# Kernel tuning notes

Measured on AMD Instinct MI355X. Metric: run time of the kernel, lower is better.

## Reference

```python
import jax, jax.numpy as jnp
import numpy as np

V, E, H, B, S = 50000, 300, 512, 32, 400
SENT_STEP = 20

def _seg_matrix(seq_len, step):
    # PyTorch default: boundaries = range(0, S, step), append S-1 if missing.
    bounds = list(range(0, seq_len, step))
    if bounds[-1] != seq_len - 1:
        bounds.append(seq_len - 1)
    seg = np.searchsorted(np.array(bounds), np.arange(seq_len))  # token -> sentence id
    M = np.zeros((seq_len, len(bounds)), np.float32)
    M[np.arange(seq_len), seg] = 1.0
    M /= M.sum(0, keepdims=True)  # column-normalized -> segment MEAN pooling
    return jnp.asarray(M)

SEG_M = _seg_matrix(S, SENT_STEP)  # [S, n_sent] = [400, 21]

def _gru_dir(x_proj, w_hh, b_hh, reverse):
    # x_proj: [B,T,3H] precomputed x @ W_ih^T + b_ih. PyTorch gate order: r, z, n.
    def step(h, xp):
        gh = h @ w_hh.T + b_hh
        xr, xz, xn = jnp.split(xp, 3, axis=-1)
        hr, hz, hn = jnp.split(gh, 3, axis=-1)
        r = jax.nn.sigmoid(xr + hr)
        z = jax.nn.sigmoid(xz + hz)
        n = jnp.tanh(xn + r * hn)
        h2 = (1.0 - z) * n + z * h
        return h2, h2
    h0 = jnp.zeros((x_proj.shape[0], w_hh.shape[1]), x_proj.dtype)
    h_last, outs = jax.lax.scan(step, h0, x_proj.transpose(1, 0, 2), reverse=reverse)
    return h_last, outs.transpose(1, 0, 2)  # [B,H], [B,T,H]

def _bigru(x, wif, whf, bif, bhf, wib, whb, bib, bhb):
    hf, of = _gru_dir(x @ wif.T + bif, whf, bhf, False)
    hb, ob = _gru_dir(x @ wib.T + bib, whb, bhb, True)
    return jnp.concatenate([of, ob], -1), hf, hb

def setup_inputs():
    key = jax.random.key(0)
    ks = jax.random.split(key, 20)
    f = lambda k, shp: jax.random.normal(k, shp, jnp.float32) * 0.1
    return {
        'input_seq': jax.random.randint(ks[0], (B, S), 0, V),
        'emb': f(ks[1], (V, E)),
        'w_ih_wf': f(ks[2], (3 * H, E)), 'w_hh_wf': f(ks[3], (3 * H, H)),
        'b_ih_wf': f(ks[4], (3 * H,)), 'b_hh_wf': f(ks[5], (3 * H,)),
        'w_ih_wb': f(ks[6], (3 * H, E)), 'w_hh_wb': f(ks[7], (3 * H, H)),
        'b_ih_wb': f(ks[8], (3 * H,)), 'b_hh_wb': f(ks[9], (3 * H,)),
        'w_ih_sf': f(ks[10], (3 * H, 2 * H)), 'w_hh_sf': f(ks[11], (3 * H, H)),
        'b_ih_sf': f(ks[12], (3 * H,)), 'b_hh_sf': f(ks[13], (3 * H,)),
        'w_ih_sb': f(ks[14], (3 * H, 2 * H)), 'w_hh_sb': f(ks[15], (3 * H, H)),
        'b_ih_sb': f(ks[16], (3 * H,)), 'b_hh_sb': f(ks[17], (3 * H,)),
        'fc_w': f(ks[18], (H, 2 * H)), 'fc_b': f(ks[19], (H,)),
    }

def reference(input_seq, emb, w_ih_wf, w_hh_wf, b_ih_wf, b_hh_wf,
              w_ih_wb, w_hh_wb, b_ih_wb, b_hh_wb,
              w_ih_sf, w_hh_sf, b_ih_sf, b_hh_sf,
              w_ih_sb, w_hh_sb, b_ih_sb, b_hh_sb, fc_w, fc_b):
    x = emb[input_seq]  # [B,S,E]; dropout is identity in eval mode
    word_out, _, _ = _bigru(x, w_ih_wf, w_hh_wf, b_ih_wf, b_hh_wf,
                            w_ih_wb, w_hh_wb, b_ih_wb, b_hh_wb)  # [B,S,2H]
    # fused ragged segment-mean pooling (replaces the double python loop)
    sent_rep = jnp.einsum('btd,ts->bsd', word_out, SEG_M)  # [B,n_sent,2H]
    sent_out, hf, hb = _bigru(sent_rep, w_ih_sf, w_hh_sf, b_ih_sf, b_hh_sf,
                              w_ih_sb, w_hh_sb, b_ih_sb, b_hh_sb)
    hidden = jnp.concatenate([hf, hb], -1) @ fc_w.T + fc_b  # [B,H]
    return sent_out, hidden
```

## Files before the change

### kernel.cpp

```cpp
#include <hip/hip_runtime.h>
#include <hip/hip_bf16.h>
#include <hip/hip_cooperative_groups.h>

typedef __bf16 bf16;
typedef __bf16 bf16x4 __attribute__((ext_vector_type(4)));
typedef __bf16 bf16x8 __attribute__((ext_vector_type(8)));
typedef float f32x4 __attribute__((ext_vector_type(4)));

static __device__ __forceinline__ bf16 f2b(float x) { return (bf16)x; }
static __device__ __forceinline__ float b2f(bf16 x) { return (float)x; }

static __device__ __forceinline__ f32x4 mfma16(bf16x8 a, bf16x8 b, f32x4 c) {
  return __builtin_amdgcn_mfma_f32_16x16x32_bf16(a, b, c, 0, 0, 0);
}

static __device__ __forceinline__ bf16x8 loadb8_cc(const bf16* p) {
  bf16x8 v;
  asm volatile("global_load_dwordx4 %0, %1, off sc0 sc1" : "=v"(v) : "v"(p) : "memory");
  return v;
}
static __device__ __forceinline__ void store_b16_cc(bf16* p, bf16 v) {
  unsigned short s;
  __builtin_memcpy(&s, &v, 2);
  unsigned u = s;
  asm volatile("global_store_short %0, %1, off sc0 sc1" :: "v"(p), "v"(u) : "memory");
}

__global__ __launch_bounds__(256) void pad_gather_cvt(
    const float* __restrict__ src, bf16* __restrict__ dst,
    const int* __restrict__ seq, int nrows) {
  int row = blockIdx.x * 4 + (threadIdx.x >> 6);
  int lane = threadIdx.x & 63;
  if (row >= nrows) return;
  int srow;
  if (seq) {
    int s = row >> 5, b = row & 31;
    srow = seq[b * 400 + s];
  } else {
    srow = row;
  }
  const float* sp = src + (size_t)srow * 300;
  bf16* dp = dst + (size_t)row * 320;
  for (int i = lane; i < 320; i += 64) dp[i] = (i < 300) ? f2b(sp[i]) : (bf16)0.f;
}

__global__ __launch_bounds__(256) void cvt_f32_bf16(const float* __restrict__ src,
                                                    bf16* __restrict__ dst,
                                                    int n4) {
  int i = blockIdx.x * 256 + threadIdx.x;
  int stride = gridDim.x * 256;
  for (; i < n4; i += stride) {
    float4 v = ((const float4*)src)[i];
    bf16x4 o = {f2b(v.x), f2b(v.y), f2b(v.z), f2b(v.w)};
    *(bf16x4*)(dst + (size_t)i * 4) = o;
  }
}

__global__ __launch_bounds__(256) void gemm_bt_al(const float* __restrict__ A,
                                                  const bf16* __restrict__ W,
                                                  const float* __restrict__ bias,
                                                  float* __restrict__ C,
                                                  int M, int N, int K) {
  __shared__ bf16 AsH[128][72];
  __shared__ bf16 AsL[128][72];
  __shared__ bf16 Ws[128][72];
  const int n0 = blockIdx.x * 128, m0 = blockIdx.y * 128;
  const int tid = threadIdx.x;
  const int wave = tid >> 6, lane = tid & 63;
  const int l15 = lane & 15, lq = lane >> 4;
  const int wm = (wave >> 1) * 64, wn = (wave & 1) * 64;

  f32x4 acc[4][4] = {};

  for (int k0 = 0; k0 < K; k0 += 64) {
    __syncthreads();
#pragma unroll
    for (int i = 0; i < 8; ++i) {
      int c = tid + 256 * i;
      int r = c >> 4, cc = (c & 15) * 4;
      int gr = m0 + r;
      float4 v = {0.f, 0.f, 0.f, 0.f};
      if (gr < M) v = *(const float4*)(A + (size_t)gr * K + k0 + cc);
      float vv[4] = {v.x, v.y, v.z, v.w};
#pragma unroll
      for (int j = 0; j < 4; ++j) {
        bf16 h = f2b(vv[j]);
        AsH[r][cc + j] = h;
        AsL[r][cc + j] = f2b(vv[j] - b2f(h));
      }
    }
#pragma unroll
    for (int i = 0; i < 4; ++i) {
      int c = tid + 256 * i;
      int r = c >> 3, cc = (c & 7) * 8;
      *(bf16x8*)&Ws[r][cc] = *(const bf16x8*)(W + (size_t)(n0 + r) * K + k0 + cc);
    }
    __syncthreads();
#pragma unroll
    for (int ks = 0; ks < 64; ks += 32) {
      bf16x8 afH[4], afL[4], bfr[4];
#pragma unroll
      for (int i = 0; i < 4; ++i) {
        afH[i] = *(const bf16x8*)&AsH[wm + i * 16 + l15][ks + lq * 8];
        afL[i] = *(const bf16x8*)&AsL[wm + i * 16 + l15][ks + lq * 8];
      }
#pragma unroll
      for (int j = 0; j < 4; ++j)
        bfr[j] = *(const bf16x8*)&Ws[wn + j * 16 + l15][ks + lq * 8];
#pragma unroll
      for (int i = 0; i < 4; ++i)
#pragma unroll
        for (int j = 0; j < 4; ++j) {
          acc[i][j] = mfma16(afH[i], bfr[j], acc[i][j]);
          acc[i][j] = mfma16(afL[i], bfr[j], acc[i][j]);
        }
    }
  }

#pragma unroll
  for (int i = 0; i < 4; ++i)
#pragma unroll
    for (int j = 0; j < 4; ++j) {
      int col = n0 + wn + j * 16 + l15;
      float bv = bias[col];
#pragma unroll
      for (int r = 0; r < 4; ++r) {
        int row = m0 + wm + i * 16 + lq * 4 + r;
        if (row < M) C[(size_t)row * N + col] = acc[i][j][r] + bv;
      }
    }
}

__global__ __launch_bounds__(256) void gru_word(
    const float* __restrict__ whhF, const float* __restrict__ whhB,
    const float* __restrict__ bhhF, const float* __restrict__ bhhB,
    const float* __restrict__ bihF, const float* __restrict__ bihB,
    const bf16* __restrict__ wpad,
    const bf16* __restrict__ xpad,
    bf16* __restrict__ hexb,
    unsigned* __restrict__ flags,
    float* __restrict__ srep)
{
  __shared__ bf16 WlH[48][516];
  __shared__ bf16 WlL[48][516];
  __shared__ bf16 Xw[48][324];
  __shared__ float red[2][4][64][4];
  const int tid = threadIdx.x;
  const int bx = blockIdx.x;
  const int dir = bx >> 5, nb = bx & 31;
  const int c0 = nb * 16;
  const float* whh = dir ? whhB : whhF;
  const float* bhh = dir ? bhhB : bhhF;
  const float* bih = dir ? bihB : bihF;
  const bf16* wih = wpad + (size_t)dir * 1536 * 320;
  unsigned* flg = flags + dir * 32;

#pragma unroll
  for (int i = 0; i < 24; ++i) {
    int c = tid + 256 * i;
    int r = c >> 7, kc = (c & 127) * 4;
    int gr = ((r >> 4) << 9) + c0 + (r & 15);
    float4 v = *(const float4*)(whh + (size_t)gr * 512 + kc);
    float vv[4] = {v.x, v.y, v.z, v.w};
#pragma unroll
    for (int j = 0; j < 4; ++j) {
      bf16 h = f2b(vv[j]);
      WlH[r][kc + j] = h;
      WlL[r][kc + j] = f2b(vv[j] - b2f(h));
    }
  }
#pragma unroll
  for (int i = 0; i < 8; ++i) {
    int c = tid + 256 * i;
    if (c < 1920) {
      int r = c / 40, ch = (c % 40) * 8;
      int gr = ((r >> 4) << 9) + c0 + (r & 15);
      *(bf16x8*)&Xw[r][ch] = *(const bf16x8*)(wih + (size_t)gr * 320 + ch);
    }
  }
  __syncthreads();

  const int wave = tid >> 6, lane = tid & 63;
  const int kh = wave >> 1;
  const int mh = wave & 1;
  const int m0 = mh * 16;
  const int l15 = lane & 15, lq = lane >> 4;
  const int colg = c0 + l15;
  const int rowq = m0 + lq * 4;
  const float bhr = bhh[colg];
  const float bhz = bhh[512 + colg];
  const float bhn = bhh[1024 + colg];
  const float bir = bih[colg];
  const float biz = bih[512 + colg];
  const float bin_ = bih[1024 + colg];

  float pacc0 = 0.f, pacc1 = 0.f, pacc2 = 0.f, pacc3 = 0.f;
  float hp_reg[4] = {0.f, 0.f, 0.f, 0.f};
  bf16* hex_d = hexb + (size_t)dir * 2 * 2 * 16384;

  for (int it = 0; it < 400; ++it) {
    const int t = dir ? (399 - it) : it;
    f32x4 accR = {}, accZ = {}, xN = {}, hN = {};

    {
      const bf16* xrow = xpad + (size_t)(t * 32 + m0 + l15) * 320;
      const int kb = kh * 160;
#pragma unroll
      for (int k0 = 0; k0 < 160; k0 += 32) {
        const int kk = kb + k0 + lq * 8;
        bf16x8 a = *(const bf16x8*)(xrow + kk);
        accR = mfma16(a, *(const bf16x8*)&Xw[l15][kk], accR);
        accZ = mfma16(a, *(const bf16x8*)&Xw[16 + l15][kk], accZ);
        xN = mfma16(a, *(const bf16x8*)&Xw[32 + l15][kk], xN);
      }
    }

    if (it > 0) {
      if (tid < 32) {
        while (__hip_atomic_load(&flg[tid], __ATOMIC_RELAXED,
                                 __HIP_MEMORY_SCOPE_AGENT) < (unsigned)it)
          __builtin_amdgcn_s_sleep(1);
      }
      __syncthreads();

      const bf16* hH = hex_d + (size_t)((it - 1) & 1) * 2 * 16384;
      const bf16* hL = hH + 16384;
      const int rowoff = (m0 + l15) * 512 + kh * 256 + lq * 8;
      bf16x8 hiA[8], loA[8];
#pragma unroll
      for (int c = 0; c < 8; ++c) {
        hiA[c] = loadb8_cc(hH + rowoff + c * 32);
        loA[c] = loadb8_cc(hL + rowoff + c * 32);
      }
      asm volatile("s_waitcnt vmcnt(0)" ::: "memory");
      __builtin_amdgcn_sched_barrier(0);

#pragma unroll
      for (int c = 0; c < 8; ++c) {
        const int kk = kh * 256 + c * 32 + lq * 8;
        bf16x8 wrh = *(const bf16x8*)&WlH[l15][kk];
        bf16x8 wrl = *(const bf16x8*)&WlL[l15][kk];
        bf16x8 wzh = *(const bf16x8*)&WlH[16 + l15][kk];
        bf16x8 wzl = *(const bf16x8*)&WlL[16 + l15][kk];
        bf16x8 wnh = *(const bf16x8*)&WlH[32 + l15][kk];
        bf16x8 wnl = *(const bf16x8*)&WlL[32 + l15][kk];
        accR = mfma16(hiA[c], wrh, accR);
        accR = mfma16(loA[c], wrh, accR);
        accR = mfma16(hiA[c], wrl, accR);
        accZ = mfma16(hiA[c], wzh, accZ);
        accZ = mfma16(loA[c], wzh, accZ);
        accZ = mfma16(hiA[c], wzl, accZ);
        hN = mfma16(hiA[c], wnh, hN);
        hN = mfma16(loA[c], wnh, hN);
        hN = mfma16(hiA[c], wnl, hN);
      }
    }

    if (kh == 0) {
      *(f32x4*)&red[mh][0][lane][0] = accR;
      *(f32x4*)&red[mh][1][lane][0] = accZ;
      *(f32x4*)&red[mh][2][lane][0] = xN;
      *(f32x4*)&red[mh][3][lane][0] = hN;
    }
    __syncthreads();
    if (kh == 1) {
      accR = accR + *(const f32x4*)&red[mh][0][lane][0];
      accZ = accZ + *(const f32x4*)&red[mh][1][lane][0];
      xN = xN + *(const f32x4*)&red[mh][2][lane][0];
      hN = hN + *(const f32x4*)&red[mh][3][lane][0];

      bf16* dH = hex_d + (size_t)(it & 1) * 2 * 16384;
      bf16* dL = dH + 16384;
      float h2v[4];
#pragma unroll
      for (int r = 0; r < 4; ++r) {
        int b = rowq + r;
        float rr = 1.f / (1.f + expf(-(accR[r] + bir + bhr)));
        float zz = 1.f / (1.f + expf(-(accZ[r] + biz + bhz)));
        float nn = tanhf(xN[r] + bin_ + rr * (hN[r] + bhn));
        h2v[r] = (1.f - zz) * nn + zz * hp_reg[r];
        hp_reg[r] = h2v[r];
        bf16 hi = f2b(h2v[r]);
        bf16 lo = f2b(h2v[r] - b2f(hi));
        store_b16_cc(dH + (b << 9) + colg, hi);
        store_b16_cc(dL + (b << 9) + colg, lo);
      }

      int sg = (t == 0) ? 0 : ((t + 19) / 20);
      if (sg > 20) sg = 20;
      float ic = (sg == 0) ? 1.0f : (sg == 20 ? (1.0f / 19.0f) : 0.05f);
      pacc0 += h2v[0] * ic; pacc1 += h2v[1] * ic;
      pacc2 += h2v[2] * ic; pacc3 += h2v[3] * ic;
      bool flush = dir ? (t == 0 || (t % 20) == 1) : ((t % 20) == 0 || t == 399);
      if (flush) {
        float* sp = srep + ((size_t)(sg * 32 + rowq) * 1024) + (dir << 9) + colg;
        sp[0] = pacc0; sp[1024] = pacc1;
        sp[2048] = pacc2; sp[3072] = pacc3;
        pacc0 = pacc1 = pacc2 = pacc3 = 0.f;
      }
    }

    asm volatile("s_waitcnt vmcnt(0)" ::: "memory");
    __syncthreads();
    if (tid == 0)
      __hip_atomic_store(&flg[nb], (unsigned)(it + 1), __ATOMIC_RELAXED,
                         __HIP_MEMORY_SCOPE_AGENT);
  }
}

__global__ __launch_bounds__(256) void gru_sent(
    const float* __restrict__ whhF, const float* __restrict__ whhB,
    const float* __restrict__ bhhF, const float* __restrict__ bhhB,
    const float* __restrict__ xproj,
    bf16* __restrict__ hexb,
    unsigned* __restrict__ flags,
    float* __restrict__ out,
    float* __restrict__ hfin)
{
  __shared__ bf16 WlH[48][516];
  __shared__ bf16 WlL[48][516];
  __shared__ float red[2][3][64][4];
  const int tid = threadIdx.x;
  const int bx = blockIdx.x;
  const int dir = bx >> 5, nb = bx & 31;
  const int c0 = nb * 16;
  const float* whh = dir ? whhB : whhF;
  const float* bhh = dir ? bhhB : bhhF;
  unsigned* flg = flags + dir * 32;

#pragma unroll
  for (int i = 0; i < 24; ++i) {
    int c = tid + 256 * i;
    int r = c >> 7, kc = (c & 127) * 4;
    int gr = ((r >> 4) << 9) + c0 + (r & 15);
    float4 v = *(const float4*)(whh + (size_t)gr * 512 + kc);
    float vv[4] = {v.x, v.y, v.z, v.w};
#pragma unroll
    for (int j = 0; j < 4; ++j) {
      bf16 h = f2b(vv[j]);
      WlH[r][kc + j] = h;
      WlL[r][kc + j] = f2b(vv[j] - b2f(h));
    }
  }
  __syncthreads();

  const int wave = tid >> 6, lane = tid & 63;
  const int kh = wave >> 1;
  const int mh = wave & 1;
  const int m0 = mh * 16;
  const int l15 = lane & 15, lq = lane >> 4;
  const int colg = c0 + l15;
  const int rowq = m0 + lq * 4;
  const float bhr = bhh[colg];
  const float bhz = bhh[512 + colg];
  const float bhn = bhh[1024 + colg];

  float hp_reg[4] = {0.f, 0.f, 0.f, 0.f};
  bf16* hex_d = hexb + (size_t)dir * 2 * 2 * 16384;

  for (int it = 0; it < 21; ++it) {
    const int t = dir ? (20 - it) : it;
    f32x4 accR = {}, accZ = {}, hN = {};

    if (it > 0) {
      if (tid < 32) {
        while (__hip_atomic_load(&flg[tid], __ATOMIC_RELAXED,
                                 __HIP_MEMORY_SCOPE_AGENT) < (unsigned)it)
          __builtin_amdgcn_s_sleep(1);
      }
      __syncthreads();

      const bf16* hH = hex_d + (size_t)((it - 1) & 1) * 2 * 16384;
      const bf16* hL = hH + 16384;
      const int rowoff = (m0 + l15) * 512 + kh * 256 + lq * 8;
      bf16x8 hiA[8], loA[8];
#pragma unroll
      for (int c = 0; c < 8; ++c) {
        hiA[c] = loadb8_cc(hH + rowoff + c * 32);
        loA[c] = loadb8_cc(hL + rowoff + c * 32);
      }
      asm volatile("s_waitcnt vmcnt(0)" ::: "memory");
      __builtin_amdgcn_sched_barrier(0);

#pragma unroll
      for (int c = 0; c < 8; ++c) {
        const int kk = kh * 256 + c * 32 + lq * 8;
        bf16x8 wrh = *(const bf16x8*)&WlH[l15][kk];
        bf16x8 wrl = *(const bf16x8*)&WlL[l15][kk];
        bf16x8 wzh = *(const bf16x8*)&WlH[16 + l15][kk];
        bf16x8 wzl = *(const bf16x8*)&WlL[16 + l15][kk];
        bf16x8 wnh = *(const bf16x8*)&WlH[32 + l15][kk];
        bf16x8 wnl = *(const bf16x8*)&WlL[32 + l15][kk];
        accR = mfma16(hiA[c], wrh, accR);
        accR = mfma16(loA[c], wrh, accR);
        accR = mfma16(hiA[c], wrl, accR);
        accZ = mfma16(hiA[c], wzh, accZ);
        accZ = mfma16(loA[c], wzh, accZ);
        accZ = mfma16(hiA[c], wzl, accZ);
        hN = mfma16(hiA[c], wnh, hN);
        hN = mfma16(loA[c], wnh, hN);
        hN = mfma16(hiA[c], wnl, hN);
      }
    }

    if (kh == 0) {
      *(f32x4*)&red[mh][0][lane][0] = accR;
      *(f32x4*)&red[mh][1][lane][0] = accZ;
      *(f32x4*)&red[mh][2][lane][0] = hN;
    }
    __syncthreads();
    if (kh == 1) {
      accR = accR + *(const f32x4*)&red[mh][0][lane][0];
      accZ = accZ + *(const f32x4*)&red[mh][1][lane][0];
      hN = hN + *(const f32x4*)&red[mh][2][lane][0];

      const float* xp = xproj + ((size_t)dir * 672 + t * 32) * 1536;
      bf16* dH = hex_d + (size_t)(it & 1) * 2 * 16384;
      bf16* dL = dH + 16384;
#pragma unroll
      for (int r = 0; r < 4; ++r) {
        int b = rowq + r;
        float xr = xp[b * 1536 + colg];
        float xz = xp[b * 1536 + 512 + colg];
        float xn = xp[b * 1536 + 1024 + colg];
        float rr = 1.f / (1.f + expf(-(xr + accR[r] + bhr)));
        float zz = 1.f / (1.f + expf(-(xz + accZ[r] + bhz)));
        float nn = tanhf(xn + rr * (hN[r] + bhn));
        float h2 = (1.f - zz) * nn + zz * hp_reg[r];
        hp_reg[r] = h2;
        bf16 hi = f2b(h2);
        bf16 lo = f2b(h2 - b2f(hi));
        store_b16_cc(dH + (b << 9) + colg, hi);
        store_b16_cc(dL + (b << 9) + colg, lo);
        out[(size_t)b * (21 * 1024) + (size_t)t * 1024 + (dir << 9) + colg] = h2;
        if (it == 20) hfin[(dir << 14) + b * 512 + colg] = h2;
      }
    }

    asm volatile("s_waitcnt vmcnt(0)" ::: "memory");
    __syncthreads();
    if (tid == 0)
      __hip_atomic_store(&flg[nb], (unsigned)(it + 1), __ATOMIC_RELAXED,
                         __HIP_MEMORY_SCOPE_AGENT);
  }
}

__global__ __launch_bounds__(256) void fc_k(const float* __restrict__ hfin,
                                            const float* __restrict__ fcw,
                                            const float* __restrict__ fcb,
                                            float* __restrict__ out) {
  __shared__ float hl[1024];
  int b = blockIdx.x, tid = threadIdx.x;
  for (int i = tid; i < 512; i += 256) {
    hl[i] = hfin[b * 512 + i];
    hl[512 + i] = hfin[16384 + b * 512 + i];
  }
  __syncthreads();
  for (int j = tid; j < 512; j += 256) {
    const float* wr = fcw + (size_t)j * 1024;
    float acc = 0.f;
    for (int k = 0; k < 1024; k += 4) {
      float4 wv = *(const float4*)(wr + k);
      acc += hl[k] * wv.x + hl[k + 1] * wv.y + hl[k + 2] * wv.z +
             hl[k + 3] * wv.w;
    }
    out[688128 + b * 512 + j] = acc + fcb[j];
  }
}

extern "C" void kernel_launch(void* const* d_in, const int* in_sizes, int n_in,
                              void* d_out, int out_size, void* d_ws,
                              size_t ws_size, hipStream_t stream) {
  const int* seq = (const int*)d_in[0];
  const float* emb = (const float*)d_in[1];
  const float* w_ih_wf = (const float*)d_in[2];
  const float* w_hh_wf = (const float*)d_in[3];
  const float* b_ih_wf = (const float*)d_in[4];
  const float* b_hh_wf = (const float*)d_in[5];
  const float* w_ih_wb = (const float*)d_in[6];
  const float* w_hh_wb = (const float*)d_in[7];
  const float* b_ih_wb = (const float*)d_in[8];
  const float* b_hh_wb = (const float*)d_in[9];
  const float* w_ih_sf = (const float*)d_in[10];
  const float* w_hh_sf = (const float*)d_in[11];
  const float* b_ih_sf = (const float*)d_in[12];
  const float* b_hh_sf = (const float*)d_in[13];
  const float* w_ih_sb = (const float*)d_in[14];
  const float* w_hh_sb = (const float*)d_in[15];
  const float* b_ih_sb = (const float*)d_in[16];
  const float* b_hh_sb = (const float*)d_in[17];
  const float* fc_w = (const float*)d_in[18];
  const float* fc_b = (const float*)d_in[19];

  char* ws = (char*)d_ws;
  bf16* xpad = (bf16*)(ws + 0);
  bf16* wpadw = (bf16*)(ws + 8192000);
  bf16* wihs = (bf16*)(ws + 10158080);
  float* srep = (float*)(ws + 16449536);
  float* xps = (float*)(ws + 19202048);
  bf16* hexb = (bf16*)(ws + 27459584);
  float* hfin = (float*)(ws + 27721728);
  unsigned* flags = (unsigned*)(ws + 27852800);

  hipMemsetAsync(ws + 16449536, 0, 27854848 - 16449536, stream);

  pad_gather_cvt<<<3200, 256, 0, stream>>>(emb, xpad, seq, 12800);
  pad_gather_cvt<<<384, 256, 0, stream>>>(w_ih_wf, wpadw, nullptr, 1536);
  pad_gather_cvt<<<384, 256, 0, stream>>>(w_ih_wb, wpadw + 1536 * 320, nullptr,
                                          1536);
  cvt_f32_bf16<<<1536, 256, 0, stream>>>(w_ih_sf, wihs, 393216);
  cvt_f32_bf16<<<1536, 256, 0, stream>>>(w_ih_sb, wihs + 1572864, 393216);

  {
    unsigned* flgW = flags;
    void* args[] = {(void*)&w_hh_wf, (void*)&w_hh_wb, (void*)&b_hh_wf,
                    (void*)&b_hh_wb, (void*)&b_ih_wf, (void*)&b_ih_wb,
                    (void*)&wpadw,   (void*)&xpad,    (void*)&hexb,
                    (void*)&flgW,    (void*)&srep};
    hipLaunchCooperativeKernel((const void*)gru_word, dim3(64), dim3(256),
                               args, 0, stream);
  }

  dim3 g2(12, 6);
  gemm_bt_al<<<g2, 256, 0, stream>>>(srep, wihs, b_ih_sf, xps, 672, 1536, 1024);
  gemm_bt_al<<<g2, 256, 0, stream>>>(srep, wihs + 1572864, b_ih_sb,
                                     xps + (size_t)672 * 1536, 672, 1536, 1024);

  {
    unsigned* flgS = flags + 128;
    float* outp = (float*)d_out;
    const float* xpsc = xps;
    void* args[] = {(void*)&w_hh_sf, (void*)&w_hh_sb, (void*)&b_hh_sf,
                    (void*)&b_hh_sb, (void*)&xpsc,    (void*)&hexb,
                    (void*)&flgS,    (void*)&outp,    (void*)&hfin};
    hipLaunchCooperativeKernel((const void*)gru_sent, dim3(64), dim3(256),
                               args, 0, stream);
  }

  fc_k<<<32, 256, 0, stream>>>(hfin, fc_w, fc_b, (float*)d_out);
}
```

Before: 2.781 ms.

## Stage hidden-state exchange in LDS and write contiguous per-block tiles

```diff
diff --git a/kernel.cpp b/kernel.cpp
--- a/kernel.cpp
+++ b/kernel.cpp
@@ -19,11 +19,8 @@
   asm volatile("global_load_dwordx4 %0, %1, off sc0 sc1" : "=v"(v) : "v"(p) : "memory");
   return v;
 }
-static __device__ __forceinline__ void store_b16_cc(bf16* p, bf16 v) {
-  unsigned short s;
-  __builtin_memcpy(&s, &v, 2);
-  unsigned u = s;
-  asm volatile("global_store_short %0, %1, off sc0 sc1" :: "v"(p), "v"(u) : "memory");
+static __device__ __forceinline__ void storeb8_cc(bf16* p, bf16x8 v) {
+  asm volatile("global_store_dwordx4 %0, %1, off sc0 sc1" :: "v"(p), "v"(v) : "memory");
 }
 
 __global__ __launch_bounds__(256) void pad_gather_cvt(
@@ -145,6 +142,7 @@
   __shared__ bf16 WlL[48][516];
   __shared__ bf16 Xw[48][324];
   __shared__ float red[2][4][64][4];
+  __shared__ __align__(16) bf16 stg[2][32][16];
   const int tid = threadIdx.x;
   const int bx = blockIdx.x;
   const int dir = bx >> 5, nb = bx & 31;
@@ -187,6 +185,9 @@
   const int l15 = lane & 15, lq = lane >> 4;
   const int colg = c0 + l15;
   const int rowq = m0 + lq * 4;
+  const int arow = m0 + l15;
+  const int nboff = lq >> 1;
+  const int coff = (lq & 1) * 8;
   const float bhr = bhh[colg];
   const float bhz = bhh[512 + colg];
   const float bhn = bhh[1024 + colg];
@@ -196,14 +197,14 @@
 
   float pacc0 = 0.f, pacc1 = 0.f, pacc2 = 0.f, pacc3 = 0.f;
   float hp_reg[4] = {0.f, 0.f, 0.f, 0.f};
-  bf16* hex_d = hexb + (size_t)dir * 2 * 2 * 16384;
+  bf16* hex_d = hexb + (size_t)dir * 32768 * 2;
 
   for (int it = 0; it < 400; ++it) {
     const int t = dir ? (399 - it) : it;
     f32x4 accR = {}, accZ = {}, xN = {}, hN = {};
 
     {
-      const bf16* xrow = xpad + (size_t)(t * 32 + m0 + l15) * 320;
+      const bf16* xrow = xpad + (size_t)(t * 32 + arow) * 320;
       const int kb = kh * 160;
 #pragma unroll
       for (int k0 = 0; k0 < 160; k0 += 32) {
@@ -223,14 +224,14 @@
       }
       __syncthreads();
 
-      const bf16* hH = hex_d + (size_t)((it - 1) & 1) * 2 * 16384;
-      const bf16* hL = hH + 16384;
-      const int rowoff = (m0 + l15) * 512 + kh * 256 + lq * 8;
+      const bf16* hb = hex_d + (size_t)((it - 1) & 1) * 32768;
+      const int inrow = arow * 16 + coff;
       bf16x8 hiA[8], loA[8];
 #pragma unroll
       for (int c = 0; c < 8; ++c) {
-        hiA[c] = loadb8_cc(hH + rowoff + c * 32);
-        loA[c] = loadb8_cc(hL + rowoff + c * 32);
+        const bf16* ph = hb + (size_t)(kh * 16 + c * 2 + nboff) * 1024 + inrow;
+        hiA[c] = loadb8_cc(ph);
+        loA[c] = loadb8_cc(ph + 512);
       }
       asm volatile("s_waitcnt vmcnt(0)" ::: "memory");
       __builtin_amdgcn_sched_barrier(0);
@@ -269,8 +270,6 @@
       xN = xN + *(const f32x4*)&red[mh][2][lane][0];
       hN = hN + *(const f32x4*)&red[mh][3][lane][0];
 
-      bf16* dH = hex_d + (size_t)(it & 1) * 2 * 16384;
-      bf16* dL = dH + 16384;
       float h2v[4];
 #pragma unroll
       for (int r = 0; r < 4; ++r) {
@@ -281,9 +280,8 @@
         h2v[r] = (1.f - zz) * nn + zz * hp_reg[r];
         hp_reg[r] = h2v[r];
         bf16 hi = f2b(h2v[r]);
-        bf16 lo = f2b(h2v[r] - b2f(hi));
-        store_b16_cc(dH + (b << 9) + colg, hi);
-        store_b16_cc(dL + (b << 9) + colg, lo);
+        stg[0][b][l15] = hi;
+        stg[1][b][l15] = f2b(h2v[r] - b2f(hi));
       }
 
       int sg = (t == 0) ? 0 : ((t + 19) / 20);
@@ -300,6 +298,11 @@
       }
     }
 
+    __syncthreads();
+    if (tid < 128) {
+      bf16* dst = hex_d + (size_t)(it & 1) * 32768 + (size_t)nb * 1024;
+      storeb8_cc(dst + tid * 8, ((const bf16x8*)&stg[0][0][0])[tid]);
+    }
     asm volatile("s_waitcnt vmcnt(0)" ::: "memory");
     __syncthreads();
     if (tid == 0)
@@ -320,6 +323,7 @@
   __shared__ bf16 WlH[48][516];
   __shared__ bf16 WlL[48][516];
   __shared__ float red[2][3][64][4];
+  __shared__ __align__(16) bf16 stg[2][32][16];
   const int tid = threadIdx.x;
   const int bx = blockIdx.x;
   const int dir = bx >> 5, nb = bx & 31;
@@ -351,12 +355,15 @@
   const int l15 = lane & 15, lq = lane >> 4;
   const int colg = c0 + l15;
   const int rowq = m0 + lq * 4;
+  const int arow = m0 + l15;
+  const int nboff = lq >> 1;
+  const int coff = (lq & 1) * 8;
   const float bhr = bhh[colg];
   const float bhz = bhh[512 + colg];
   const float bhn = bhh[1024 + colg];
 
   float hp_reg[4] = {0.f, 0.f, 0.f, 0.f};
-  bf16* hex_d = hexb + (size_t)dir * 2 * 2 * 16384;
+  bf16* hex_d = hexb + (size_t)dir * 32768 * 2;
 
   for (int it = 0; it < 21; ++it) {
     const int t = dir ? (20 - it) : it;
@@ -370,14 +377,14 @@
       }
       __syncthreads();
 
-      const bf16* hH = hex_d + (size_t)((it - 1) & 1) * 2 * 16384;
-      const bf16* hL = hH + 16384;
-      const int rowoff = (m0 + l15) * 512 + kh * 256 + lq * 8;
+      const bf16* hb = hex_d + (size_t)((it - 1) & 1) * 32768;
+      const int inrow = arow * 16 + coff;
       bf16x8 hiA[8], loA[8];
 #pragma unroll
       for (int c = 0; c < 8; ++c) {
-        hiA[c] = loadb8_cc(hH + rowoff + c * 32);
-        loA[c] = loadb8_cc(hL + rowoff + c * 32);
+        const bf16* ph = hb + (size_t)(kh * 16 + c * 2 + nboff) * 1024 + inrow;
+        hiA[c] = loadb8_cc(ph);
+        loA[c] = loadb8_cc(ph + 512);
       }
       asm volatile("s_waitcnt vmcnt(0)" ::: "memory");
       __builtin_amdgcn_sched_barrier(0);
@@ -415,8 +422,6 @@
       hN = hN + *(const f32x4*)&red[mh][2][lane][0];
 
       const float* xp = xproj + ((size_t)dir * 672 + t * 32) * 1536;
-      bf16* dH = hex_d + (size_t)(it & 1) * 2 * 16384;
-      bf16* dL = dH + 16384;
 #pragma unroll
       for (int r = 0; r < 4; ++r) {
         int b = rowq + r;
@@ -429,14 +434,18 @@
         float h2 = (1.f - zz) * nn + zz * hp_reg[r];
         hp_reg[r] = h2;
         bf16 hi = f2b(h2);
-        bf16 lo = f2b(h2 - b2f(hi));
-        store_b16_cc(dH + (b << 9) + colg, hi);
-        store_b16_cc(dL + (b << 9) + colg, lo);
+        stg[0][b][l15] = hi;
+        stg[1][b][l15] = f2b(h2 - b2f(hi));
         out[(size_t)b * (21 * 1024) + (size_t)t * 1024 + (dir << 9) + colg] = h2;
         if (it == 20) hfin[(dir << 14) + b * 512 + colg] = h2;
       }
     }
 
+    __syncthreads();
+    if (tid < 128) {
+      bf16* dst = hex_d + (size_t)(it & 1) * 32768 + (size_t)nb * 1024;
+      storeb8_cc(dst + tid * 8, ((const bf16x8*)&stg[0][0][0])[tid]);
+    }
     asm volatile("s_waitcnt vmcnt(0)" ::: "memory");
     __syncthreads();
     if (tid == 0)
```

Result: faster. 2.309 ms (-17.0%).
